# Optimization experiments

Measured on AMD Instinct MI355X. Metric: run time of the kernel, lower is better.

Reference implementation:

```python
import jax, jax.numpy as jnp
import numpy as np

H = 8        # num_heads
D = 768      # d_model
DH = D // H  # d_head = 96


def setup_inputs() -> dict:
    key = jax.random.key(0)
    ks = jax.random.split(key, 12)
    B, S = 4, 2048
    s_in = 1.0 / np.sqrt(D)
    s_cat = 1.0 / np.sqrt(D)
    return {
        "input_querys": jax.random.normal(ks[0], (B, S, D), jnp.float32),
        "input_key": jax.random.normal(ks[1], (B, S, D), jnp.float32),
        "input_values": jax.random.normal(ks[2], (B, S, D), jnp.float32),
        # per-head projection weights, stacked over the head axis
        "Wq": jax.random.normal(ks[3], (H, D, DH), jnp.float32) * s_in,
        "bq": jax.random.normal(ks[4], (H, DH), jnp.float32) * s_in,
        "Wk": jax.random.normal(ks[5], (H, D, DH), jnp.float32) * s_in,
        "bk": jax.random.normal(ks[6], (H, DH), jnp.float32) * s_in,
        "Wv": jax.random.normal(ks[7], (H, D, DH), jnp.float32) * s_in,
        "bv": jax.random.normal(ks[8], (H, DH), jnp.float32) * s_in,
        # output linear: (H*DH) -> D
        "Wo": jax.random.normal(ks[9], (H * DH, D), jnp.float32) * s_cat,
        "bo": jax.random.normal(ks[10], (D,), jnp.float32) * s_cat,
    }


def reference(input_querys, input_key, input_values, Wq, bq, Wk, bk, Wv, bv, Wo, bo):
    # Per-head linear projections (vectorized over the head axis)
    # q/k/v: [B,S,D] -> [B,H,S,DH]
    Q = jnp.einsum("bsd,hdk->bhsk", input_querys, Wq) + bq[None, :, None, :]
    K = jnp.einsum("bsd,hdk->bhsk", input_key, Wk) + bk[None, :, None, :]
    V = jnp.einsum("bsd,hdk->bhsk", input_values, Wv) + bv[None, :, None, :]

    scale = 1.0 / jnp.sqrt(jnp.asarray(DH, Q.dtype))
    scores = jnp.einsum("bhsk,bhtk->bhst", Q, K) * scale  # [B,H,S,S]
    attn = jax.nn.softmax(scores, axis=-1)
    out = jnp.einsum("bhst,bhtk->bhsk", attn, V)  # [B,H,S,DH]

    # concat heads (head-major order matches torch.cat over ModuleList)
    B, _, S, _ = out.shape
    cat = out.transpose(0, 2, 1, 3).reshape(B, S, H * DH)
    return cat @ Wo + bo
```

## Files before the change

kernel.cpp:

```cpp
#include <hip/hip_runtime.h>


typedef unsigned short u16;
typedef _Float16 h16;
typedef h16 h16x8 __attribute__((ext_vector_type(8)));
typedef __fp16 fp16x2 __attribute__((ext_vector_type(2)));
typedef unsigned short u16x8 __attribute__((ext_vector_type(8)));
typedef unsigned short u16x4 __attribute__((ext_vector_type(4)));
typedef float f32x4 __attribute__((ext_vector_type(4)));

__device__ __forceinline__ u16 f2h(float f) {
  union { h16 h; u16 u; } c; c.h = (h16)f; return c.u;
}

__device__ __forceinline__ void gll16(const void* g, void* l) {
  __builtin_amdgcn_global_load_lds(
      (const __attribute__((address_space(1))) void*)g,
      (__attribute__((address_space(3))) void*)l, 16, 0, 0);
}

__global__ __launch_bounds__(256) void prep_kernel(
    const float* __restrict__ Wq, const float* __restrict__ Wk,
    const float* __restrict__ Wv, const float* __restrict__ Wo,
    const float* __restrict__ Xk, const float* __restrict__ Xv,
    const float* __restrict__ Xq,
    u16* __restrict__ WqT, u16* __restrict__ WkT,
    u16* __restrict__ WvT, u16* __restrict__ WoT,
    u16* __restrict__ Xk16, u16* __restrict__ Xv16, u16* __restrict__ Xq16)
{
  const long gid = (long)blockIdx.x * 256 + threadIdx.x;
  if (gid >= 294912) {
    long i = gid - 294912;
    const int t = (int)(i / 786432);
    const long e = (i % 786432) * 8;
    const float* src = (t == 0) ? Xk : (t == 1) ? Xv : Xq;
    u16* dst = (t == 0) ? Xk16 : (t == 1) ? Xv16 : Xq16;
    f32x4 a = *(const f32x4*)(&src[e]);
    f32x4 b = *(const f32x4*)(&src[e + 4]);
    u16x8 v;
    #pragma unroll
    for (int j = 0; j < 4; j++) { v[j] = f2h(a[j]); v[4 + j] = f2h(b[j]); }
    *(u16x8*)(&dst[e]) = v;
    return;
  }
  int idx = (int)gid * 8;
  int region = idx / 589824;
  int i = idx % 589824;
  int n = i / 768;
  int d = i % 768;
  u16x8 v;
  if (region == 3) {
    #pragma unroll
    for (int j = 0; j < 8; j++) v[j] = f2h(Wo[(size_t)(d + j) * 768 + n]);
    *(u16x8*)(&WoT[i]) = v;
  } else {
    int h = n / 96, kk = n % 96;
    const float* W = (region == 0) ? Wq : (region == 1) ? Wk : Wv;
    u16* T = (region == 0) ? WqT : (region == 1) ? WkT : WvT;
    #pragma unroll
    for (int j = 0; j < 8; j++) v[j] = f2h(W[(size_t)h * 73728 + (size_t)(d + j) * 96 + kk]);
    *(u16x8*)(&T[i]) = v;
  }
}

#define GK 768

__global__ __launch_bounds__(256) void gemm_qkv(
    const float* __restrict__ XqF, const u16* __restrict__ Xq16,
    const u16* __restrict__ Xk16, const u16* __restrict__ Xv16,
    const u16* __restrict__ WT,
    const float* __restrict__ bq, const float* __restrict__ bk,
    const float* __restrict__ bv,
    u16* __restrict__ Q16, u16* __restrict__ K16, u16* __restrict__ VT,
    int qfp32)
{
  const int z = blockIdx.z;
  const u16* BT = WT + (size_t)z * 589824;
  const float* bias = (z == 0) ? bq : (z == 1) ? bk : bv;

  __shared__ __align__(16) u16 As[128 * 32];
  __shared__ __align__(16) u16 Bs[64 * 32];
  const int tid = threadIdx.x;
  const int wave = tid >> 6;
  const int lane = tid & 63;
  const int quad = lane >> 4;
  const int l16 = lane & 15;
  const int m0 = blockIdx.x * 128;
  const int n0 = blockIdx.y * 64;

  f32x4 acc[2][4];
  #pragma unroll
  for (int i = 0; i < 2; i++)
    #pragma unroll
    for (int j = 0; j < 4; j++) acc[i][j] = (f32x4){0.f, 0.f, 0.f, 0.f};

  if (z == 0 && qfp32) {
    const float* A = XqF;
    const int ar = tid >> 2;
    const int ac = (tid & 3) * 8;

    f32x4 pf[4];
    u16x8 pb;
    {
      pf[0] = *(const f32x4*)(&A[(size_t)(m0 + ar) * GK + ac]);
      pf[1] = *(const f32x4*)(&A[(size_t)(m0 + ar) * GK + ac + 4]);
      pf[2] = *(const f32x4*)(&A[(size_t)(m0 + 64 + ar) * GK + ac]);
      pf[3] = *(const f32x4*)(&A[(size_t)(m0 + 64 + ar) * GK + ac + 4]);
      pb = *(const u16x8*)(&BT[(size_t)(n0 + ar) * GK + ac]);
    }

    for (int kt = 0; kt < 24; kt++) {
      u16x8 h0, h1;
      #pragma unroll
      for (int j = 0; j < 4; j++) {
        h0[j] = f2h(pf[0][j]); h0[4 + j] = f2h(pf[1][j]);
        h1[j] = f2h(pf[2][j]); h1[4 + j] = f2h(pf[3][j]);
      }
      *(u16x8*)(&As[ar * 32 + ac]) = h0;
      *(u16x8*)(&As[(64 + ar) * 32 + ac]) = h1;
      *(u16x8*)(&Bs[ar * 32 + ac]) = pb;
      __syncthreads();

      if (kt + 1 < 24) {
        const int k0 = (kt + 1) * 32;
        pf[0] = *(const f32x4*)(&A[(size_t)(m0 + ar) * GK + k0 + ac]);
        pf[1] = *(const f32x4*)(&A[(size_t)(m0 + ar) * GK + k0 + ac + 4]);
        pf[2] = *(const f32x4*)(&A[(size_t)(m0 + 64 + ar) * GK + k0 + ac]);
        pf[3] = *(const f32x4*)(&A[(size_t)(m0 + 64 + ar) * GK + k0 + ac + 4]);
        pb = *(const u16x8*)(&BT[(size_t)(n0 + ar) * GK + k0 + ac]);
      }

      h16x8 af[2], bf[4];
      #pragma unroll
      for (int mf = 0; mf < 2; mf++)
        af[mf] = *(const h16x8*)(&As[(wave * 32 + mf * 16 + l16) * 32 + quad * 8]);
      #pragma unroll
      for (int nf = 0; nf < 4; nf++)
        bf[nf] = *(const h16x8*)(&Bs[(nf * 16 + l16) * 32 + quad * 8]);
      #pragma unroll
      for (int mf = 0; mf < 2; mf++)
        #pragma unroll
        for (int nf = 0; nf < 4; nf++)
          acc[mf][nf] = __builtin_amdgcn_mfma_f32_16x16x32_f16(af[mf], bf[nf], acc[mf][nf], 0, 0, 0);

      if (kt + 1 < 24) __syncthreads();
    }
  } else {
    const u16* A = (z == 0) ? Xq16 : (z == 1) ? Xk16 : Xv16;
    const int Lr = lane >> 2, Lc = (lane & 3) * 8;
    const u16* gA0 = A + (size_t)(m0 + wave * 32 + Lr) * GK + Lc;
    const u16* gA1 = gA0 + (size_t)16 * GK;
    const u16* gB  = BT + (size_t)(n0 + wave * 16 + Lr) * GK + Lc;
    u16* lA0 = &As[(wave * 32) * 32];
    u16* lA1 = &As[(wave * 32 + 16) * 32];
    u16* lB  = &Bs[(wave * 16) * 32];

    for (int kt = 0; kt < 24; kt++) {
      gll16(gA0, lA0);
      gll16(gA1, lA1);
      gll16(gB, lB);
      gA0 += 32; gA1 += 32; gB += 32;
      __syncthreads();

      h16x8 af[2], bf[4];
      #pragma unroll
      for (int mf = 0; mf < 2; mf++)
        af[mf] = *(const h16x8*)(&As[(wave * 32 + mf * 16 + l16) * 32 + quad * 8]);
      #pragma unroll
      for (int nf = 0; nf < 4; nf++)
        bf[nf] = *(const h16x8*)(&Bs[(nf * 16 + l16) * 32 + quad * 8]);
      #pragma unroll
      for (int mf = 0; mf < 2; mf++)
        #pragma unroll
        for (int nf = 0; nf < 4; nf++)
          acc[mf][nf] = __builtin_amdgcn_mfma_f32_16x16x32_f16(af[mf], bf[nf], acc[mf][nf], 0, 0, 0);
      __syncthreads();
    }
  }

  u16* Yr = (z == 0) ? Q16 : K16;
  #pragma unroll
  for (int nf = 0; nf < 4; nf++) {
    const int n = n0 + nf * 16 + l16;
    const float bv2 = bias[n];
    #pragma unroll
    for (int mf = 0; mf < 2; mf++) {
      const int m = m0 + wave * 32 + mf * 16 + quad * 4;
      if (z == 2) {
        const int b = m >> 11, s = m & 2047;
        u16x4 pk;
        #pragma unroll
        for (int r = 0; r < 4; r++) pk[r] = f2h(acc[mf][nf][r] + bv2);
        *(u16x4*)(&VT[(size_t)b * 768 * 2048 + (size_t)n * 2048 + s]) = pk;
      } else {
        #pragma unroll
        for (int r = 0; r < 4; r++)
          Yr[(size_t)(m + r) * GK + n] = f2h(acc[mf][nf][r] + bv2);
      }
    }
  }
}

__global__ __launch_bounds__(256) void gemm_o(
    const u16* __restrict__ A, const u16* __restrict__ BT,
    const float* __restrict__ bias, float* __restrict__ Y)
{
  __shared__ __align__(16) u16 As[128 * 32];
  __shared__ __align__(16) u16 Bs[64 * 32];
  const int tid = threadIdx.x;
  const int wave = tid >> 6;
  const int lane = tid & 63;
  const int quad = lane >> 4;
  const int l16 = lane & 15;
  const int m0 = blockIdx.x * 128;
  const int n0 = blockIdx.y * 64;

  f32x4 acc[2][4];
  #pragma unroll
  for (int i = 0; i < 2; i++)
    #pragma unroll
    for (int j = 0; j < 4; j++) acc[i][j] = (f32x4){0.f, 0.f, 0.f, 0.f};

  const int Lr = lane >> 2, Lc = (lane & 3) * 8;
  const u16* gA0 = A + (size_t)(m0 + wave * 32 + Lr) * GK + Lc;
  const u16* gA1 = gA0 + (size_t)16 * GK;
  const u16* gB  = BT + (size_t)(n0 + wave * 16 + Lr) * GK + Lc;
  u16* lA0 = &As[(wave * 32) * 32];
  u16* lA1 = &As[(wave * 32 + 16) * 32];
  u16* lB  = &Bs[(wave * 16) * 32];

  for (int kt = 0; kt < 24; kt++) {
    gll16(gA0, lA0);
    gll16(gA1, lA1);
    gll16(gB, lB);
    gA0 += 32; gA1 += 32; gB += 32;
    __syncthreads();

    h16x8 af[2], bf[4];
    #pragma unroll
    for (int mf = 0; mf < 2; mf++)
      af[mf] = *(const h16x8*)(&As[(wave * 32 + mf * 16 + l16) * 32 + quad * 8]);
    #pragma unroll
    for (int nf = 0; nf < 4; nf++)
      bf[nf] = *(const h16x8*)(&Bs[(nf * 16 + l16) * 32 + quad * 8]);
    #pragma unroll
    for (int mf = 0; mf < 2; mf++)
      #pragma unroll
      for (int nf = 0; nf < 4; nf++)
        acc[mf][nf] = __builtin_amdgcn_mfma_f32_16x16x32_f16(af[mf], bf[nf], acc[mf][nf], 0, 0, 0);
    __syncthreads();
  }

  #pragma unroll
  for (int nf = 0; nf < 4; nf++) {
    const int n = n0 + nf * 16 + l16;
    const float bv = bias[n];
    #pragma unroll
    for (int mf = 0; mf < 2; mf++) {
      const int m = m0 + wave * 32 + mf * 16 + quad * 4;
      #pragma unroll
      for (int r = 0; r < 4; r++)
        Y[(size_t)(m + r) * GK + n] = acc[mf][nf][r] + bv;
    }
  }
}

#define SEQ 2048
#define LQK 104
#define LVT 72
#define LPS 72

__global__ __launch_bounds__(256) void attn_kernel(
    const u16* __restrict__ Q, const u16* __restrict__ K,
    const u16* __restrict__ VT, u16* __restrict__ O)
{
  __shared__ __align__(16) u16 Ks[64 * LQK];
  __shared__ __align__(16) u16 Vt[96 * LVT];
  __shared__ __align__(16) u16 Ps[4][32 * LPS];

  const int tid = threadIdx.x;
  const int wave = tid >> 6;
  const int lane = tid & 63;
  const int quad = lane >> 4;
  const int l16 = lane & 15;

  const int bh = blockIdx.y;
  const int b = bh >> 3, h = bh & 7;
  const int q0 = blockIdx.x * 128;

  const size_t batch_off = (size_t)b * SEQ * 768;
  const u16* Kg = K + batch_off + h * 96;
  const u16* Vg = VT + (size_t)b * 768 * 2048 + (size_t)(h * 96) * 2048;

  h16x8 qf[2][3];
  #pragma unroll
  for (int mf = 0; mf < 2; mf++) {
    const u16* Qrow = Q + batch_off +
        (size_t)(q0 + wave * 32 + mf * 16 + l16) * 768 + h * 96 + quad * 8;
    #pragma unroll
    for (int ks = 0; ks < 3; ks++) qf[mf][ks] = *(const h16x8*)(&Qrow[ks * 32]);
  }

  int krr[3], kcc[3], vrr[3], vcc[3];
  #pragma unroll
  for (int j = 0; j < 3; j++) {
    const int ik = tid + j * 256;
    krr[j] = ik / 12; kcc[j] = (ik % 12) * 8;
    vrr[j] = ik >> 3; vcc[j] = (ik & 7) * 8;
  }

  f32x4 o[2][6];
  #pragma unroll
  for (int mf = 0; mf < 2; mf++)
    #pragma unroll
    for (int i = 0; i < 6; i++) o[mf][i] = (f32x4){0.f, 0.f, 0.f, 0.f};
  float m_raw[2] = {-1e30f, -1e30f};
  float lrow[2] = {0.f, 0.f};
  const float sc = 0.14724498f;

  u16* Pw = &Ps[wave][0];

  u16x8 kA[3], vA[3];
  #pragma unroll
  for (int j = 0; j < 3; j++) {
    kA[j] = *(const u16x8*)(&Kg[(size_t)krr[j] * 768 + kcc[j]]);
    vA[j] = *(const u16x8*)(&Vg[(size_t)vrr[j] * 2048 + vcc[j]]);
  }

  for (int kt = 0; kt < SEQ / 64; kt++) {
    #pragma unroll
    for (int j = 0; j < 3; j++) {
      *(u16x8*)(&Ks[krr[j] * LQK + kcc[j]]) = kA[j];
      *(u16x8*)(&Vt[vrr[j] * LVT + vcc[j]]) = vA[j];
    }
    __syncthreads();

    if (kt + 1 < SEQ / 64) {
      const u16* Kn = Kg + (size_t)(kt + 1) * 64 * 768;
      const u16* Vn = Vg + (size_t)(kt + 1) * 64;
      #pragma unroll
      for (int j = 0; j < 3; j++) {
        kA[j] = *(const u16x8*)(&Kn[(size_t)krr[j] * 768 + kcc[j]]);
        vA[j] = *(const u16x8*)(&Vn[(size_t)vrr[j] * 2048 + vcc[j]]);
      }
    }

    f32x4 s[2][4];
    #pragma unroll
    for (int mf = 0; mf < 2; mf++)
      #pragma unroll
      for (int kf = 0; kf < 4; kf++) s[mf][kf] = (f32x4){0.f, 0.f, 0.f, 0.f};
    __builtin_amdgcn_s_setprio(1);
    #pragma unroll
    for (int ks = 0; ks < 3; ks++) {
      #pragma unroll
      for (int kf = 0; kf < 4; kf++) {
        h16x8 a = *(const h16x8*)(&Ks[(kf * 16 + l16) * LQK + ks * 32 + quad * 8]);
        s[0][kf] = __builtin_amdgcn_mfma_f32_16x16x32_f16(a, qf[0][ks], s[0][kf], 0, 0, 0);
        s[1][kf] = __builtin_amdgcn_mfma_f32_16x16x32_f16(a, qf[1][ks], s[1][kf], 0, 0, 0);
      }
    }
    __builtin_amdgcn_s_setprio(0);

    #pragma unroll
    for (int mf = 0; mf < 2; mf++) {
      float mx = s[mf][0][0];
      #pragma unroll
      for (int kf = 0; kf < 4; kf++)
        #pragma unroll
        for (int r = 0; r < 4; r++) mx = fmaxf(mx, s[mf][kf][r]);
      mx = fmaxf(mx, __shfl_xor(mx, 16));
      mx = fmaxf(mx, __shfl_xor(mx, 32));
      if (__any(mx > m_raw[mf] + 54.0f)) {
        const float mnew = fmaxf(m_raw[mf], mx);
        const float alpha = exp2f(sc * (m_raw[mf] - mnew));
        lrow[mf] *= alpha;
        #pragma unroll
        for (int nfo = 0; nfo < 6; nfo++)
          #pragma unroll
          for (int r = 0; r < 4; r++) o[mf][nfo][r] *= alpha;
        m_raw[mf] = mnew;
      }
      const float c0 = sc * m_raw[mf];
      float ps = 0.f;
      #pragma unroll
      for (int kf = 0; kf < 4; kf++)
        #pragma unroll
        for (int r = 0; r < 4; r++) {
          float p = exp2f(fmaf(s[mf][kf][r], sc, -c0));
          s[mf][kf][r] = p;
          ps += p;
        }
      lrow[mf] += ps;

      #pragma unroll
      for (int kf = 0; kf < 4; kf++)
        #pragma unroll
        for (int rp = 0; rp < 4; rp += 2) {
          fp16x2 pk = __builtin_amdgcn_cvt_pkrtz(s[mf][kf][rp], s[mf][kf][rp + 1]);
          *(fp16x2*)(&Pw[(mf * 16 + l16) * LPS + kf * 16 + quad * 4 + rp]) = pk;
        }
    }

    __builtin_amdgcn_s_setprio(1);
    #pragma unroll
    for (int ks = 0; ks < 2; ks++) {
      h16x8 pf0 = *(const h16x8*)(&Pw[l16 * LPS + ks * 32 + quad * 8]);
      h16x8 pf1 = *(const h16x8*)(&Pw[(16 + l16) * LPS + ks * 32 + quad * 8]);
      #pragma unroll
      for (int nfo = 0; nfo < 6; nfo++) {
        h16x8 vfr = *(const h16x8*)(&Vt[(nfo * 16 + l16) * LVT + ks * 32 + quad * 8]);
        o[0][nfo] = __builtin_amdgcn_mfma_f32_16x16x32_f16(vfr, pf0, o[0][nfo], 0, 0, 0);
        o[1][nfo] = __builtin_amdgcn_mfma_f32_16x16x32_f16(vfr, pf1, o[1][nfo], 0, 0, 0);
      }
    }
    __builtin_amdgcn_s_setprio(0);
    __syncthreads();
  }

  #pragma unroll
  for (int mf = 0; mf < 2; mf++) {
    float l = lrow[mf];
    l += __shfl_xor(l, 16);
    l += __shfl_xor(l, 32);
    const float inv = 1.0f / l;
    u16* Ob = O + batch_off +
        (size_t)(q0 + wave * 32 + mf * 16 + l16) * 768 + h * 96;
    #pragma unroll
    for (int nfo = 0; nfo < 6; nfo++) {
      fp16x2 lo = __builtin_amdgcn_cvt_pkrtz(o[mf][nfo][0] * inv, o[mf][nfo][1] * inv);
      fp16x2 hi = __builtin_amdgcn_cvt_pkrtz(o[mf][nfo][2] * inv, o[mf][nfo][3] * inv);
      *(fp16x2*)(&Ob[nfo * 16 + quad * 4]) = lo;
      *(fp16x2*)(&Ob[nfo * 16 + quad * 4 + 2]) = hi;
    }
  }
}

extern "C" void kernel_launch(void* const* d_in, const int* in_sizes, int n_in,
                              void* d_out, int out_size, void* d_ws, size_t ws_size,
                              hipStream_t stream) {
  const float* Xq = (const float*)d_in[0];
  const float* Xk = (const float*)d_in[1];
  const float* Xv = (const float*)d_in[2];
  const float* Wq = (const float*)d_in[3];
  const float* bq = (const float*)d_in[4];
  const float* Wk = (const float*)d_in[5];
  const float* bk = (const float*)d_in[6];
  const float* Wv = (const float*)d_in[7];
  const float* bv = (const float*)d_in[8];
  const float* Wo = (const float*)d_in[9];
  const float* bo = (const float*)d_in[10];

  u16* wsu = (u16*)d_ws;
  u16* WT   = wsu;
  u16* WoT  = wsu + 3 * 589824;
  u16* Q16  = wsu + 4 * 589824;
  u16* Xk16 = Q16 + 6291456;
  u16* Xv16 = Xk16 + 6291456;
  u16* Xq16 = Xv16 + 6291456;

  const size_t need = (size_t)(4 * 589824 + 4 * 6291456) * 2;
  const int q16 = (ws_size >= need) ? 1 : 0;
  const int nx = q16 ? 3 : 2;

  u16* outu = (u16*)d_out;
  u16* VTb = outu;
  u16* K16 = outu + 6291456;

  u16* A16 = (u16*)d_in[0];

  prep_kernel<<<1152 + 3072 * nx, 256, 0, stream>>>(
      Wq, Wk, Wv, Wo, Xk, Xv, Xq,
      WT, WT + 589824, WT + 2 * 589824, WoT, Xk16, Xv16, Xq16);
  gemm_qkv<<<dim3(64, 12, 3), 256, 0, stream>>>(
      Xq, Xq16, Xk16, Xv16, WT, bq, bk, bv, Q16, K16, VTb, q16 ? 0 : 1);
  attn_kernel<<<dim3(16, 32), 256, 0, stream>>>(Q16, K16, VTb, A16);
  gemm_o<<<dim3(64, 12), 256, 0, stream>>>(A16, WoT, bo, (float*)d_out);
}
```

Measured before the change: 301.1 us.

## Split attention over key range with 512-thread blocks and a combine pass

Attention now runs with 512-thread blocks covering 256 queries, and the key sequence is split into two halves across blockIdx.z. Each half writes fp32 partial outputs plus its row max and sum, and a new combine kernel merges them into the fp16 attention output. The goal is more blocks and waves in flight to fill the GPU, since the old 512-block grid may have underused it. The cost is extra fp32 traffic to workspace for the partials, an extra launch, and a large workspace requirement. A fallback kernel with one 16-row tile per wave runs when the workspace is too small.

Measured after the change: 372.4 us. 23.6% more time.

```diff
diff --git a/kernel.cpp b/kernel.cpp
--- a/kernel.cpp
+++ b/kernel.cpp
@@ -5,6 +5,7 @@
 typedef _Float16 h16;
 typedef h16 h16x8 __attribute__((ext_vector_type(8)));
 typedef __fp16 fp16x2 __attribute__((ext_vector_type(2)));
+typedef __fp16 fp16x4 __attribute__((ext_vector_type(4)));
 typedef unsigned short u16x8 __attribute__((ext_vector_type(8)));
 typedef unsigned short u16x4 __attribute__((ext_vector_type(4)));
 typedef float f32x4 __attribute__((ext_vector_type(4)));
@@ -270,13 +271,14 @@
 #define LVT 72
 #define LPS 72
 
-__global__ __launch_bounds__(256) void attn_kernel(
+__global__ __launch_bounds__(512, 4) void attn_split(
     const u16* __restrict__ Q, const u16* __restrict__ K,
-    const u16* __restrict__ VT, u16* __restrict__ O)
+    const u16* __restrict__ VT,
+    float* __restrict__ Op0, float* __restrict__ Op1, float* __restrict__ ML)
 {
   __shared__ __align__(16) u16 Ks[64 * LQK];
   __shared__ __align__(16) u16 Vt[96 * LVT];
-  __shared__ __align__(16) u16 Ps[4][32 * LPS];
+  __shared__ __align__(16) u16 Ps[8][32 * LPS];
 
   const int tid = threadIdx.x;
   const int wave = tid >> 6;
@@ -286,7 +288,9 @@
 
   const int bh = blockIdx.y;
   const int b = bh >> 3, h = bh & 7;
-  const int q0 = blockIdx.x * 128;
+  const int q0 = blockIdx.x * 256;
+  const int z = blockIdx.z;
+  const int kt0 = z * 16, kt1 = kt0 + 16;
 
   const size_t batch_off = (size_t)b * SEQ * 768;
   const u16* Kg = K + batch_off + h * 96;
@@ -301,13 +305,11 @@
     for (int ks = 0; ks < 3; ks++) qf[mf][ks] = *(const h16x8*)(&Qrow[ks * 32]);
   }
 
-  int krr[3], kcc[3], vrr[3], vcc[3];
-  #pragma unroll
-  for (int j = 0; j < 3; j++) {
-    const int ik = tid + j * 256;
-    krr[j] = ik / 12; kcc[j] = (ik % 12) * 8;
-    vrr[j] = ik >> 3; vcc[j] = (ik & 7) * 8;
-  }
+  const int kr0 = tid / 12, kc0 = (tid % 12) * 8;
+  const int kr1 = (tid + 512) / 12, kc1 = ((tid + 512) % 12) * 8;
+  const int vr0 = tid >> 3, vc0 = (tid & 7) * 8;
+  const int vr1 = (tid + 512) >> 3, vc1 = ((tid + 512) & 7) * 8;
+  const bool extra = tid < 256;
 
   f32x4 o[2][6];
   #pragma unroll
@@ -320,28 +322,35 @@
 
   u16* Pw = &Ps[wave][0];
 
-  u16x8 kA[3], vA[3];
-  #pragma unroll
-  for (int j = 0; j < 3; j++) {
-    kA[j] = *(const u16x8*)(&Kg[(size_t)krr[j] * 768 + kcc[j]]);
-    vA[j] = *(const u16x8*)(&Vg[(size_t)vrr[j] * 2048 + vcc[j]]);
-  }
-
-  for (int kt = 0; kt < SEQ / 64; kt++) {
-    #pragma unroll
-    for (int j = 0; j < 3; j++) {
-      *(u16x8*)(&Ks[krr[j] * LQK + kcc[j]]) = kA[j];
-      *(u16x8*)(&Vt[vrr[j] * LVT + vcc[j]]) = vA[j];
+  u16x8 kA, kB, vA, vB;
+  {
+    const u16* K0 = Kg + (size_t)kt0 * 64 * 768;
+    const u16* V0 = Vg + (size_t)kt0 * 64;
+    kA = *(const u16x8*)(&K0[(size_t)kr0 * 768 + kc0]);
+    vA = *(const u16x8*)(&V0[(size_t)vr0 * 2048 + vc0]);
+    if (extra) {
+      kB = *(const u16x8*)(&K0[(size_t)kr1 * 768 + kc1]);
+      vB = *(const u16x8*)(&V0[(size_t)vr1 * 2048 + vc1]);
+    }
+  }
+
+  for (int kt = kt0; kt < kt1; kt++) {
+    *(u16x8*)(&Ks[kr0 * LQK + kc0]) = kA;
+    *(u16x8*)(&Vt[vr0 * LVT + vc0]) = vA;
+    if (extra) {
+      *(u16x8*)(&Ks[kr1 * LQK + kc1]) = kB;
+      *(u16x8*)(&Vt[vr1 * LVT + vc1]) = vB;
     }
     __syncthreads();
 
-    if (kt + 1 < SEQ / 64) {
+    if (kt + 1 < kt1) {
       const u16* Kn = Kg + (size_t)(kt + 1) * 64 * 768;
       const u16* Vn = Vg + (size_t)(kt + 1) * 64;
-      #pragma unroll
-      for (int j = 0; j < 3; j++) {
-        kA[j] = *(const u16x8*)(&Kn[(size_t)krr[j] * 768 + kcc[j]]);
-        vA[j] = *(const u16x8*)(&Vn[(size_t)vrr[j] * 2048 + vcc[j]]);
+      kA = *(const u16x8*)(&Kn[(size_t)kr0 * 768 + kc0]);
+      vA = *(const u16x8*)(&Vn[(size_t)vr0 * 2048 + vc0]);
+      if (extra) {
+        kB = *(const u16x8*)(&Kn[(size_t)kr1 * 768 + kc1]);
+        vB = *(const u16x8*)(&Vn[(size_t)vr1 * 2048 + vc1]);
       }
     }
 
@@ -394,12 +403,12 @@
       lrow[mf] += ps;
 
       #pragma unroll
-      for (int kf = 0; kf < 4; kf++)
-        #pragma unroll
-        for (int rp = 0; rp < 4; rp += 2) {
-          fp16x2 pk = __builtin_amdgcn_cvt_pkrtz(s[mf][kf][rp], s[mf][kf][rp + 1]);
-          *(fp16x2*)(&Pw[(mf * 16 + l16) * LPS + kf * 16 + quad * 4 + rp]) = pk;
-        }
+      for (int kf = 0; kf < 4; kf++) {
+        fp16x2 a = __builtin_amdgcn_cvt_pkrtz(s[mf][kf][0], s[mf][kf][1]);
+        fp16x2 b2 = __builtin_amdgcn_cvt_pkrtz(s[mf][kf][2], s[mf][kf][3]);
+        fp16x4 w4; w4[0] = a[0]; w4[1] = a[1]; w4[2] = b2[0]; w4[3] = b2[1];
+        *(fp16x4*)(&Pw[(mf * 16 + l16) * LPS + kf * 16 + quad * 4]) = w4;
+      }
     }
 
     __builtin_amdgcn_s_setprio(1);
@@ -418,21 +427,214 @@
     __syncthreads();
   }
 
+  float* Op = (z == 0) ? Op0 : Op1;
   #pragma unroll
   for (int mf = 0; mf < 2; mf++) {
     float l = lrow[mf];
     l += __shfl_xor(l, 16);
     l += __shfl_xor(l, 32);
     const float inv = 1.0f / l;
-    u16* Ob = O + batch_off +
-        (size_t)(q0 + wave * 32 + mf * 16 + l16) * 768 + h * 96;
+    const int row = q0 + wave * 32 + mf * 16 + l16;
+    float* Ob = Op + ((size_t)b * SEQ + row) * 768 + h * 96;
     #pragma unroll
     for (int nfo = 0; nfo < 6; nfo++) {
-      fp16x2 lo = __builtin_amdgcn_cvt_pkrtz(o[mf][nfo][0] * inv, o[mf][nfo][1] * inv);
-      fp16x2 hi = __builtin_amdgcn_cvt_pkrtz(o[mf][nfo][2] * inv, o[mf][nfo][3] * inv);
-      *(fp16x2*)(&Ob[nfo * 16 + quad * 4]) = lo;
-      *(fp16x2*)(&Ob[nfo * 16 + quad * 4 + 2]) = hi;
-    }
+      f32x4 w;
+      #pragma unroll
+      for (int r = 0; r < 4; r++) w[r] = o[mf][nfo][r] * inv;
+      *(f32x4*)(&Ob[nfo * 16 + quad * 4]) = w;
+    }
+    if (quad == 0) {
+      float* mlp = ML + (((size_t)z * 32 + bh) * SEQ + row) * 2;
+      mlp[0] = m_raw[mf];
+      mlp[1] = l;
+    }
+  }
+}
+
+__global__ __launch_bounds__(256) void combine_kernel(
+    const float* __restrict__ Op0, const float* __restrict__ Op1,
+    const float* __restrict__ ML, u16* __restrict__ A16)
+{
+  const int idx = blockIdx.x * 256 + threadIdx.x;
+  const int row = idx / 96;
+  const int c8 = (idx % 96) * 8;
+  const int h = c8 / 96 + ((c8 % 96) ? 0 : 0);
+  const int hh = c8 / 96;
+  const int b = row >> 11, s = row & 2047;
+  const int bh = b * 8 + hh;
+  (void)h;
+
+  const float sc = 0.14724498f;
+  const float* ml0 = ML + (((size_t)0 * 32 + bh) * SEQ + s) * 2;
+  const float* ml1 = ML + (((size_t)1 * 32 + bh) * SEQ + s) * 2;
+  const float m0 = ml0[0], l0 = ml0[1];
+  const float m1 = ml1[0], l1 = ml1[1];
+  const float mmax = fmaxf(m0, m1);
+  const float e0 = l0 * exp2f(sc * (m0 - mmax));
+  const float e1 = l1 * exp2f(sc * (m1 - mmax));
+  const float inv = 1.0f / (e0 + e1);
+  const float w0 = e0 * inv, w1 = e1 * inv;
+
+  const size_t off = (size_t)row * 768 + c8;
+  f32x4 a0 = *(const f32x4*)(&Op0[off]);
+  f32x4 a1 = *(const f32x4*)(&Op0[off + 4]);
+  f32x4 b0 = *(const f32x4*)(&Op1[off]);
+  f32x4 b1 = *(const f32x4*)(&Op1[off + 4]);
+  u16x8 out;
+  #pragma unroll
+  for (int r = 0; r < 4; r++) {
+    out[r]     = f2h(w0 * a0[r] + w1 * b0[r]);
+    out[4 + r] = f2h(w0 * a1[r] + w1 * b1[r]);
+  }
+  *(u16x8*)(&A16[off]) = out;
+}
+
+__global__ __launch_bounds__(512, 4) void attn_r1(
+    const u16* __restrict__ Q, const u16* __restrict__ K,
+    const u16* __restrict__ VT, u16* __restrict__ O)
+{
+  __shared__ __align__(16) u16 Ks[64 * LQK];
+  __shared__ __align__(16) u16 Vt[96 * LVT];
+  __shared__ __align__(16) u16 Ps[8][16 * LPS];
+
+  const int tid = threadIdx.x;
+  const int wave = tid >> 6;
+  const int lane = tid & 63;
+  const int quad = lane >> 4;
+  const int l16 = lane & 15;
+
+  const int bh = blockIdx.y;
+  const int b = bh >> 3, h = bh & 7;
+  const int q0 = blockIdx.x * 128;
+
+  const size_t batch_off = (size_t)b * SEQ * 768;
+  const u16* Kg = K + batch_off + h * 96;
+  const u16* Vg = VT + (size_t)b * 768 * 2048 + (size_t)(h * 96) * 2048;
+
+  h16x8 qf[3];
+  {
+    const u16* Qrow = Q + batch_off + (size_t)(q0 + wave * 16 + l16) * 768 + h * 96 + quad * 8;
+    #pragma unroll
+    for (int ks = 0; ks < 3; ks++) qf[ks] = *(const h16x8*)(&Qrow[ks * 32]);
+  }
+
+  const int kr0 = tid / 12, kc0 = (tid % 12) * 8;
+  const int kr1 = (tid + 512) / 12, kc1 = ((tid + 512) % 12) * 8;
+  const int vr0 = tid >> 3, vc0 = (tid & 7) * 8;
+  const int vr1 = (tid + 512) >> 3, vc1 = ((tid + 512) & 7) * 8;
+  const bool extra = tid < 256;
+
+  f32x4 o[6];
+  #pragma unroll
+  for (int i = 0; i < 6; i++) o[i] = (f32x4){0.f, 0.f, 0.f, 0.f};
+  float m_raw = -1e30f, lrow = 0.f;
+  const float sc = 0.14724498f;
+
+  u16* Pw = &Ps[wave][0];
+
+  u16x8 kA, kB, vA, vB;
+  kA = *(const u16x8*)(&Kg[(size_t)kr0 * 768 + kc0]);
+  vA = *(const u16x8*)(&Vg[(size_t)vr0 * 2048 + vc0]);
+  if (extra) {
+    kB = *(const u16x8*)(&Kg[(size_t)kr1 * 768 + kc1]);
+    vB = *(const u16x8*)(&Vg[(size_t)vr1 * 2048 + vc1]);
+  }
+
+  for (int kt = 0; kt < SEQ / 64; kt++) {
+    *(u16x8*)(&Ks[kr0 * LQK + kc0]) = kA;
+    *(u16x8*)(&Vt[vr0 * LVT + vc0]) = vA;
+    if (extra) {
+      *(u16x8*)(&Ks[kr1 * LQK + kc1]) = kB;
+      *(u16x8*)(&Vt[vr1 * LVT + vc1]) = vB;
+    }
+    __syncthreads();
+
+    if (kt + 1 < SEQ / 64) {
+      const u16* Kn = Kg + (size_t)(kt + 1) * 64 * 768;
+      const u16* Vn = Vg + (size_t)(kt + 1) * 64;
+      kA = *(const u16x8*)(&Kn[(size_t)kr0 * 768 + kc0]);
+      vA = *(const u16x8*)(&Vn[(size_t)vr0 * 2048 + vc0]);
+      if (extra) {
+        kB = *(const u16x8*)(&Kn[(size_t)kr1 * 768 + kc1]);
+        vB = *(const u16x8*)(&Vn[(size_t)vr1 * 2048 + vc1]);
+      }
+    }
+
+    f32x4 s[4];
+    #pragma unroll
+    for (int kf = 0; kf < 4; kf++) s[kf] = (f32x4){0.f, 0.f, 0.f, 0.f};
+    __builtin_amdgcn_s_setprio(1);
+    #pragma unroll
+    for (int ks = 0; ks < 3; ks++) {
+      #pragma unroll
+      for (int kf = 0; kf < 4; kf++) {
+        h16x8 a = *(const h16x8*)(&Ks[(kf * 16 + l16) * LQK + ks * 32 + quad * 8]);
+        s[kf] = __builtin_amdgcn_mfma_f32_16x16x32_f16(a, qf[ks], s[kf], 0, 0, 0);
+      }
+    }
+    __builtin_amdgcn_s_setprio(0);
+
+    float mx = s[0][0];
+    #pragma unroll
+    for (int kf = 0; kf < 4; kf++)
+      #pragma unroll
+      for (int r = 0; r < 4; r++) mx = fmaxf(mx, s[kf][r]);
+    mx = fmaxf(mx, __shfl_xor(mx, 16));
+    mx = fmaxf(mx, __shfl_xor(mx, 32));
+    if (__any(mx > m_raw + 54.0f)) {
+      const float mnew = fmaxf(m_raw, mx);
+      const float alpha = exp2f(sc * (m_raw - mnew));
+      lrow *= alpha;
+      #pragma unroll
+      for (int nfo = 0; nfo < 6; nfo++)
+        #pragma unroll
+        for (int r = 0; r < 4; r++) o[nfo][r] *= alpha;
+      m_raw = mnew;
+    }
+    const float c0 = sc * m_raw;
+    float ps = 0.f;
+    #pragma unroll
+    for (int kf = 0; kf < 4; kf++)
+      #pragma unroll
+      for (int r = 0; r < 4; r++) {
+        float p = exp2f(fmaf(s[kf][r], sc, -c0));
+        s[kf][r] = p;
+        ps += p;
+      }
+    lrow += ps;
+
+    #pragma unroll
+    for (int kf = 0; kf < 4; kf++)
+      #pragma unroll
+      for (int rp = 0; rp < 4; rp += 2) {
+        fp16x2 pk = __builtin_amdgcn_cvt_pkrtz(s[kf][rp], s[kf][rp + 1]);
+        *(fp16x2*)(&Pw[l16 * LPS + kf * 16 + quad * 4 + rp]) = pk;
+      }
+
+    __builtin_amdgcn_s_setprio(1);
+    #pragma unroll
+    for (int ks = 0; ks < 2; ks++) {
+      h16x8 pfr = *(const h16x8*)(&Pw[l16 * LPS + ks * 32 + quad * 8]);
+      #pragma unroll
+      for (int nfo = 0; nfo < 6; nfo++) {
+        h16x8 vfr = *(const h16x8*)(&Vt[(nfo * 16 + l16) * LVT + ks * 32 + quad * 8]);
+        o[nfo] = __builtin_amdgcn_mfma_f32_16x16x32_f16(vfr, pfr, o[nfo], 0, 0, 0);
+      }
+    }
+    __builtin_amdgcn_s_setprio(0);
+    __syncthreads();
+  }
+
+  lrow += __shfl_xor(lrow, 16);
+  lrow += __shfl_xor(lrow, 32);
+  const float inv = 1.0f / lrow;
+  u16* Ob = O + batch_off + (size_t)(q0 + wave * 16 + l16) * 768 + h * 96;
+  #pragma unroll
+  for (int nfo = 0; nfo < 6; nfo++) {
+    fp16x2 lo = __builtin_amdgcn_cvt_pkrtz(o[nfo][0] * inv, o[nfo][1] * inv);
+    fp16x2 hi = __builtin_amdgcn_cvt_pkrtz(o[nfo][2] * inv, o[nfo][3] * inv);
+    *(fp16x2*)(&Ob[nfo * 16 + quad * 4]) = lo;
+    *(fp16x2*)(&Ob[nfo * 16 + quad * 4 + 2]) = hi;
   }
 }
 
@@ -459,8 +661,14 @@
   u16* Xv16 = Xk16 + 6291456;
   u16* Xq16 = Xv16 + 6291456;
 
-  const size_t need = (size_t)(4 * 589824 + 4 * 6291456) * 2;
-  const int q16 = (ws_size >= need) ? 1 : 0;
+  float* Op0 = (float*)(wsu + 8650752);
+  float* Op1 = (float*)(wsu + 21233664);
+  float* ML  = (float*)((char*)d_ws + 67633152);
+
+  const size_t need_q16   = (size_t)(4 * 589824 + 4 * 6291456) * 2;
+  const size_t need_split = 68681728ULL;
+  const int q16 = (ws_size >= need_q16) ? 1 : 0;
+  const int do_split = (ws_size >= need_split) ? 1 : 0;
   const int nx = q16 ? 3 : 2;
 
   u16* outu = (u16*)d_out;
@@ -474,6 +682,11 @@
       WT, WT + 589824, WT + 2 * 589824, WoT, Xk16, Xv16, Xq16);
   gemm_qkv<<<dim3(64, 12, 3), 256, 0, stream>>>(
       Xq, Xq16, Xk16, Xv16, WT, bq, bk, bv, Q16, K16, VTb, q16 ? 0 : 1);
-  attn_kernel<<<dim3(16, 32), 256, 0, stream>>>(Q16, K16, VTb, A16);
+  if (do_split) {
+    attn_split<<<dim3(8, 32, 2), 512, 0, stream>>>(Q16, K16, VTb, Op0, Op1, ML);
+    combine_kernel<<<3072, 256, 0, stream>>>(Op0, Op1, ML, A16);
+  } else {
+    attn_r1<<<dim3(16, 32), 512, 0, stream>>>(Q16, K16, VTb, A16);
+  }
   gemm_o<<<dim3(64, 12), 256, 0, stream>>>(A16, WoT, bo, (float*)d_out);
 }
```
